# Kernel tuning notes

Hardware: AMD Instinct MI355X
Metric: run time of the kernel (lower is better)

The kernel has to match this reference:

```python
import jax, jax.numpy as jnp
import numpy as np

N_NODES = 100000
N_EDGES = 1600000
N_GRAPHS = 64


def setup_inputs() -> dict:
    key = jax.random.key(0)
    ks = jax.random.split(key, 10)
    x = jax.random.normal(ks[0], (N_NODES, 2), jnp.float32)
    edge_index = jax.random.randint(ks[1], (2, N_EDGES), 0, N_NODES, dtype=jnp.int64)
    batch_index = jnp.sort(jax.random.randint(ks[2], (N_NODES,), 0, N_GRAPHS, dtype=jnp.int64))

    def glorot(k, shape):
        return jax.random.normal(k, shape, jnp.float32) * jnp.sqrt(2.0 / (shape[0] + shape[1]))

    return {
        "x": x,
        "edge_index": edge_index,
        "batch_index": batch_index,
        "W1": glorot(ks[3], (2, 8)),   "b1": jnp.zeros((8,), jnp.float32),
        "W2": glorot(ks[4], (8, 32)),  "b2": jnp.zeros((32,), jnp.float32),
        "W3": glorot(ks[5], (32, 128)),"b3": jnp.zeros((128,), jnp.float32),
        "Wl": glorot(ks[6], (128, 3)), "bl": jnp.zeros((3,), jnp.float32),
    }


def _gcn_conv(x, W, b, src, dst, norm, n):
    # GCNConv: linear transform, then normalized scatter-add aggregation, then bias.
    h = x @ W                                     # [N, out]
    msg = h[src] * norm[:, None]                  # [E', out] gather + scale
    agg = jax.ops.segment_sum(msg, dst, num_segments=n)
    return agg + b


def reference(x, edge_index, batch_index, W1, b1, W2, b2, W3, b3, Wl, bl):
    n = x.shape[0]
    loop = jnp.arange(n, dtype=edge_index.dtype)
    src = jnp.concatenate([edge_index[0], loop])  # add self-loops (GCNConv default)
    dst = jnp.concatenate([edge_index[1], loop])
    # symmetric normalization D^{-1/2} (A+I) D^{-1/2}
    deg = jax.ops.segment_sum(jnp.ones_like(dst, dtype=x.dtype), dst, num_segments=n)
    dis = jnp.where(deg > 0, jax.lax.rsqrt(jnp.maximum(deg, 1.0)), 0.0)
    norm = dis[src] * dis[dst]

    h = jax.nn.relu(_gcn_conv(x, W1, b1, src, dst, norm, n))
    h = jax.nn.relu(_gcn_conv(h, W2, b2, src, dst, norm, n))  # dropout is identity in eval
    h = _gcn_conv(h, W3, b3, src, dst, norm, n)               # [N, 128]
    pooled = jax.ops.segment_max(h, batch_index, num_segments=N_GRAPHS)  # global_max_pool
    logits = pooled @ Wl + bl                                  # [G, 3]
    return jax.nn.log_softmax(logits, axis=1)
```

## Files before the change

### kernel.cpp

```cpp
#include <hip/hip_runtime.h>
#include <hip/hip_fp16.h>


#define BSHIFT 9
#define BSZ 512
#define P2_TILE 2048
#define P1_BLOCKS 128
#define SRCMASK 0x1FFFF
#define NB3 32

__device__ __forceinline__ unsigned fenc(float x) {
  unsigned b = __float_as_uint(x);
  return (b & 0x80000000u) ? ~b : (b | 0x80000000u);
}
__device__ __forceinline__ float fdec(unsigned k) {
  return (k & 0x80000000u) ? __uint_as_float(k ^ 0x80000000u)
                           : __uint_as_float(~k);
}
__device__ __forceinline__ unsigned pack2(float a, float b) {
  __half2 h = __floats2half2_rn(a, b);
  return *reinterpret_cast<unsigned*>(&h);
}
__device__ __forceinline__ float2 unpack2(unsigned u) {
  __half2 h = *reinterpret_cast<__half2*>(&u);
  return __half22float2(h);
}


__global__ __launch_bounds__(256) void p1_hist_kernel(const int* __restrict__ dst,
                                                      int* __restrict__ hist2d, int E) {
  __shared__ int h[256];
  h[threadIdx.x] = 0;
  __syncthreads();
  for (int e = blockIdx.x * blockDim.x + threadIdx.x; e < E; e += gridDim.x * blockDim.x)
    atomicAdd(&h[dst[e] >> BSHIFT], 1);
  __syncthreads();
  hist2d[blockIdx.x * 256 + threadIdx.x] = h[threadIdx.x];
}

__global__ __launch_bounds__(256) void p1_scan_kernel(const int* __restrict__ hist2d,
                                                      int* __restrict__ bucketBase,
                                                      int* __restrict__ bucketCursor,
                                                      unsigned* __restrict__ pooled,
                                                      int B, int E, int G) {
  __shared__ int s[256];
  int t = threadIdx.x;
  int v = 0;
  for (int b = 0; b < P1_BLOCKS; ++b) v += hist2d[b * 256 + t];
  if (t >= B) v = 0;
  s[t] = v;
  __syncthreads();
  for (int o = 1; o < 256; o <<= 1) {
    int u = (t >= o) ? s[t - o] : 0;
    __syncthreads();
    s[t] += u;
    __syncthreads();
  }
  int excl = s[t] - v;
  bucketBase[t] = excl;
  bucketCursor[t] = excl;
  if (t == 0) bucketBase[256] = E;
  for (int i = t; i < G * 128; i += 256) pooled[i] = 0u;
}

__global__ __launch_bounds__(256) void p2_partition_kernel(
    const int* __restrict__ src, const int* __restrict__ dst,
    int* __restrict__ bucketCursor, unsigned* __restrict__ part, int E) {
  __shared__ int hist[256];
  __shared__ int lbase[256];
  __shared__ int gbase[256];
  __shared__ int cur[256];
  __shared__ unsigned sbuf[P2_TILE];
  __shared__ unsigned abuf[P2_TILE];
  int t = threadIdx.x;
  int e0 = blockIdx.x * P2_TILE;
  int cnt = min(P2_TILE, E - e0);

  hist[t] = 0;
  __syncthreads();

  int myb[P2_TILE / 256];
  unsigned myp[P2_TILE / 256];
#pragma unroll
  for (int k = 0; k < P2_TILE / 256; ++k) {
    int i = t + k * 256;
    if (i < cnt) {
      int e = e0 + i;
      int d = dst[e];
      int b = d >> BSHIFT;
      myb[k] = b;
      myp[k] = ((unsigned)(d & (BSZ - 1)) << 17) | (unsigned)src[e];
      atomicAdd(&hist[b], 1);
    } else {
      myb[k] = -1;
      myp[k] = 0;
    }
  }
  __syncthreads();

  int v = hist[t];
  lbase[t] = v;
  __syncthreads();
  for (int o = 1; o < 256; o <<= 1) {
    int u = (t >= o) ? lbase[t - o] : 0;
    __syncthreads();
    lbase[t] += u;
    __syncthreads();
  }
  int excl = lbase[t] - v;
  __syncthreads();
  lbase[t] = excl;
  if (v > 0) gbase[t] = atomicAdd(&bucketCursor[t], v);
  cur[t] = 0;
  __syncthreads();

#pragma unroll
  for (int k = 0; k < P2_TILE / 256; ++k) {
    int b = myb[k];
    if (b >= 0) {
      int pos = atomicAdd(&cur[b], 1);
      int li = lbase[b] + pos;
      sbuf[li] = myp[k];
      abuf[li] = (unsigned)(gbase[b] + pos);
    }
  }
  __syncthreads();

#pragma unroll
  for (int k = 0; k < P2_TILE / 256; ++k) {
    int i = t + k * 256;
    if (i < cnt) part[abuf[i]] = sbuf[i];
  }
}

__global__ __launch_bounds__(512) void p3_build_kernel(
    const unsigned* __restrict__ part, const int* __restrict__ bucketBase,
    const float* __restrict__ x, unsigned* __restrict__ xsh,
    float* __restrict__ dis, int* __restrict__ rp, unsigned* __restrict__ csr,
    int N, int B, int E) {
  __shared__ int hist[BSZ];
  __shared__ int scn[BSZ];
  int b = blockIdx.x, t = threadIdx.x;
  int base = bucketBase[b], end = bucketBase[b + 1];
  int cnt = end - base;

  hist[t] = 0;
  __syncthreads();
  for (int i = t; i < cnt; i += BSZ) atomicAdd(&hist[part[base + i] >> 17], 1);
  __syncthreads();

  int v = hist[t];
  scn[t] = v;
  __syncthreads();
  for (int o = 1; o < BSZ; o <<= 1) {
    int u = (t >= o) ? scn[t - o] : 0;
    __syncthreads();
    scn[t] += u;
    __syncthreads();
  }
  int excl = scn[t] - v;

  int n = (b << BSHIFT) + t;
  if (n < N) {
    float dn = rsqrtf((float)v + 1.0f);
    dis[n] = dn;
    rp[n] = base + excl;
    float2 xn = *reinterpret_cast<const float2*>(x + 2 * (size_t)n);
    xsh[n] = pack2(dn * xn.x, dn * xn.y);
  }
  if (b == B - 1 && t == 0) rp[N] = E;

  hist[t] = excl;
  __syncthreads();
  for (int i = t; i < cnt; i += BSZ) {
    unsigned p = part[base + i];
    int pos = atomicAdd(&hist[p >> 17], 1);
    csr[base + pos] = p & SRCMASK;
  }
}


__global__ __launch_bounds__(256) void layer1_kernel(
    const int* __restrict__ rp, const unsigned* __restrict__ csr, const float* __restrict__ dis,
    const unsigned* __restrict__ xsh, const float* __restrict__ W1, const float* __restrict__ b1,
    uint4* __restrict__ h1h, int N) {
  __shared__ float sW[16];
  __shared__ float sb[8];
  int t = threadIdx.x;
  if (t < 16) sW[t] = W1[t];
  if (t < 8) sb[t] = b1[t];
  __syncthreads();
  int n = blockIdx.x * blockDim.x + t;
  if (n >= N) return;
  float2 a = unpack2(xsh[n]);
  int j0 = rp[n], j1 = rp[n + 1];
#pragma unroll 4
  for (int j = j0; j < j1; ++j) {
    const float2 v = unpack2(xsh[csr[j]]);
    a.x += v.x;
    a.y += v.y;
  }
  float dn = dis[n];
  float ax = dn * a.x, ay = dn * a.y;
  uint4 pk;
  unsigned* pw = &pk.x;
#pragma unroll
  for (int fc = 0; fc < 4; ++fc) {
    float e0 = dn * fmaxf(ax * sW[fc * 2 + 0] + ay * sW[8 + fc * 2 + 0] + sb[fc * 2 + 0], 0.f);
    float e1 = dn * fmaxf(ax * sW[fc * 2 + 1] + ay * sW[8 + fc * 2 + 1] + sb[fc * 2 + 1], 0.f);
    pw[fc] = pack2(e0, e1);
  }
  h1h[n] = pk;
}

__global__ __launch_bounds__(256) void layer2_kernel(
    const int* __restrict__ rp, const unsigned* __restrict__ csr, const float* __restrict__ dis,
    const uint4* __restrict__ h1h, const float* __restrict__ W2, const float* __restrict__ b2,
    __half* __restrict__ h2h, int N) {
  __shared__ float sW[256];
  __shared__ float sb[32];
  int t = threadIdx.x;
  sW[t] = W2[t];
  if (t < 32) sb[t] = b2[t];
  __syncthreads();
  int n = blockIdx.x * blockDim.x + t;
  if (n >= N) return;
  float acc[8];
  {
    uint4 sv = h1h[n];
    float2 f0 = unpack2(sv.x), f1 = unpack2(sv.y), f2 = unpack2(sv.z), f3 = unpack2(sv.w);
    acc[0] = f0.x; acc[1] = f0.y; acc[2] = f1.x; acc[3] = f1.y;
    acc[4] = f2.x; acc[5] = f2.y; acc[6] = f3.x; acc[7] = f3.y;
  }
  int j0 = rp[n], j1 = rp[n + 1];
#pragma unroll 4
  for (int j = j0; j < j1; ++j) {
    uint4 v = h1h[csr[j]];
    float2 g0 = unpack2(v.x), g1 = unpack2(v.y), g2 = unpack2(v.z), g3 = unpack2(v.w);
    acc[0] += g0.x; acc[1] += g0.y; acc[2] += g1.x; acc[3] += g1.y;
    acc[4] += g2.x; acc[5] += g2.y; acc[6] += g3.x; acc[7] += g3.y;
  }
  float dn = dis[n];
#pragma unroll
  for (int k = 0; k < 8; ++k) acc[k] *= dn;
  uint4 pk[4];
  unsigned* pw = &pk[0].x;
#pragma unroll
  for (int fc = 0; fc < 8; ++fc) {
    float4 o;
    o.x = sb[fc * 4 + 0]; o.y = sb[fc * 4 + 1]; o.z = sb[fc * 4 + 2]; o.w = sb[fc * 4 + 3];
#pragma unroll
    for (int k = 0; k < 8; ++k) {
      const float4 w = *reinterpret_cast<const float4*>(&sW[k * 32 + fc * 4]);
      float a = acc[k];
      o.x += a * w.x; o.y += a * w.y; o.z += a * w.z; o.w += a * w.w;
    }
    o.x = dn * fmaxf(o.x, 0.f);
    o.y = dn * fmaxf(o.y, 0.f);
    o.z = dn * fmaxf(o.z, 0.f);
    o.w = dn * fmaxf(o.w, 0.f);
    pw[fc * 2 + 0] = pack2(o.x, o.y);
    pw[fc * 2 + 1] = pack2(o.z, o.w);
  }
  uint4* dst16 = reinterpret_cast<uint4*>(h2h + (size_t)n * 32);
  dst16[0] = pk[0];
  dst16[1] = pk[1];
  dst16[2] = pk[2];
  dst16[3] = pk[3];
}

__global__ __launch_bounds__(128) void layer3_pool_kernel(
    const int* __restrict__ rp, const unsigned* __restrict__ csr, const float* __restrict__ dis,
    const __half* __restrict__ h2h, const float* __restrict__ W3, const float* __restrict__ b3,
    const int* __restrict__ batch, unsigned* __restrict__ pooled, int N) {
  __shared__ float rows[NB3][32];
  __shared__ float dnv[NB3];
  int t = threadIdx.x;
  int gi = t >> 2;
  int q = t & 3;

  int n0 = blockIdx.x * NB3;
  int m = min(NB3, N - n0);

  if (t < m) dnv[t] = dis[n0 + t];

  if (gi < m) {
    int n = n0 + gi;
    uint4 sv = *reinterpret_cast<const uint4*>(h2h + (size_t)n * 32 + q * 8);
    float2 f0 = unpack2(sv.x), f1 = unpack2(sv.y), f2 = unpack2(sv.z), f3 = unpack2(sv.w);
    float acc[8] = {f0.x, f0.y, f1.x, f1.y, f2.x, f2.y, f3.x, f3.y};
    int j0 = rp[n], j1 = rp[n + 1];
#pragma unroll 4
    for (int j = j0; j < j1; ++j) {
      int s = csr[j];
      uint4 v = *reinterpret_cast<const uint4*>(h2h + (size_t)s * 32 + q * 8);
      float2 g0 = unpack2(v.x), g1 = unpack2(v.y), g2 = unpack2(v.z), g3 = unpack2(v.w);
      acc[0] += g0.x; acc[1] += g0.y; acc[2] += g1.x; acc[3] += g1.y;
      acc[4] += g2.x; acc[5] += g2.y; acc[6] += g3.x; acc[7] += g3.y;
    }
#pragma unroll
    for (int i = 0; i < 8; ++i) rows[gi][q * 8 + i] = acc[i];
  }
  __syncthreads();

  float Wreg[32];
#pragma unroll
  for (int k = 0; k < 32; ++k) Wreg[k] = W3[k * 128 + t];
  float bb = b3[t];

  int curg = batch[n0];
  float runmax = -INFINITY;
  for (int r = 0; r < m; ++r) {
    int g = batch[n0 + r];
    if (g != curg) {
      atomicMax(&pooled[(size_t)curg * 128 + t], fenc(runmax));
      runmax = -INFINITY;
      curg = g;
    }
    float acc = 0.f;
#pragma unroll
    for (int k = 0; k < 32; ++k) acc += rows[r][k] * Wreg[k];
    runmax = fmaxf(runmax, dnv[r] * acc + bb);
  }
  atomicMax(&pooled[(size_t)curg * 128 + t], fenc(runmax));
}

__global__ __launch_bounds__(128) void head_kernel(
    const unsigned* __restrict__ pooled, const float* __restrict__ Wl,
    const float* __restrict__ bl, float* __restrict__ out, int G) {
  int g = blockIdx.x;
  int t = threadIdx.x;
  float p = fdec(pooled[(size_t)g * 128 + t]);
  __shared__ float red[128];
  __shared__ float sj[3];
  for (int j = 0; j < 3; ++j) {
    red[t] = p * Wl[t * 3 + j];
    __syncthreads();
    for (int k = 64; k > 0; k >>= 1) {
      if (t < k) red[t] += red[t + k];
      __syncthreads();
    }
    if (t == 0) sj[j] = red[0];
    __syncthreads();
  }
  if (t == 0) {
    float l0 = sj[0] + bl[0], l1 = sj[1] + bl[1], l2 = sj[2] + bl[2];
    float m = fmaxf(l0, fmaxf(l1, l2));
    float lse = logf(expf(l0 - m) + expf(l1 - m) + expf(l2 - m));
    out[g * 3 + 0] = l0 - m - lse;
    out[g * 3 + 1] = l1 - m - lse;
    out[g * 3 + 2] = l2 - m - lse;
  }
}

extern "C" void kernel_launch(void* const* d_in, const int* in_sizes, int n_in,
                              void* d_out, int out_size, void* d_ws, size_t ws_size,
                              hipStream_t stream) {
  const float* x = (const float*)d_in[0];
  const int* ei = (const int*)d_in[1];
  const int* batch = (const int*)d_in[2];
  const float* W1 = (const float*)d_in[3];
  const float* b1 = (const float*)d_in[4];
  const float* W2 = (const float*)d_in[5];
  const float* b2 = (const float*)d_in[6];
  const float* W3 = (const float*)d_in[7];
  const float* b3 = (const float*)d_in[8];
  const float* Wl = (const float*)d_in[9];
  const float* bl = (const float*)d_in[10];
  float* out = (float*)d_out;

  const int N = in_sizes[0] / 2;
  const int E = in_sizes[1] / 2;
  const int G = out_size / 3;

  const int* src = ei;
  const int* dstp = ei + E;

  const int B = (N + BSZ - 1) / BSZ;

  size_t NP = ((size_t)N + 256) & ~(size_t)255;
  size_t EP = ((size_t)E + 255) & ~(size_t)255;

  float* dis = (float*)d_ws;
  int* rp = (int*)d_ws + NP;
  unsigned* csr = (unsigned*)(rp + NP);
  unsigned* part = (unsigned*)(csr + EP);
  int* bucketBase = (int*)(part + EP);
  int* bucketCursor = bucketBase + 512;
  int* hist2d = bucketCursor + 512;
  float* arena = (float*)(hist2d + P1_BLOCKS * 256);

  unsigned* xsh = (unsigned*)arena;
  uint4* h1h = (uint4*)(arena + (size_t)N);
  __half* h2h = (__half*)(arena + (size_t)5 * N);
  unsigned* pooled = (unsigned*)(arena + (size_t)21 * N);

  const int BS = 256;
  auto cdiv = [](long long a, long long b) { return (int)((a + b - 1) / b); };

  p1_hist_kernel<<<P1_BLOCKS, 256, 0, stream>>>(dstp, hist2d, E);
  p1_scan_kernel<<<1, 256, 0, stream>>>(hist2d, bucketBase, bucketCursor, pooled, B, E, G);
  p2_partition_kernel<<<cdiv(E, P2_TILE), 256, 0, stream>>>(src, dstp, bucketCursor, part, E);
  p3_build_kernel<<<B, BSZ, 0, stream>>>(part, bucketBase, x, xsh, dis, rp, csr, N, B, E);

  layer1_kernel<<<cdiv(N, BS), BS, 0, stream>>>(rp, csr, dis, xsh, W1, b1, h1h, N);
  layer2_kernel<<<cdiv(N, BS), BS, 0, stream>>>(rp, csr, dis, h1h, W2, b2, h2h, N);
  layer3_pool_kernel<<<cdiv(N, NB3), 128, 0, stream>>>(rp, csr, dis, h2h, W3, b3, batch, pooled, N);

  head_kernel<<<G, 128, 0, stream>>>(pooled, Wl, bl, out, G);
}
```

Baseline: 134.1 us.

## Sort nodes by degree within each bucket to balance warp work in layers 1-2

The CSR build kernel now computes a per-bucket counting sort of nodes by in-degree (capped at 63) and writes a permutation array. Layers 1 and 2 process nodes in that permuted order so that lanes in a wavefront have similar neighbor-loop trip counts, reducing divergence from uneven degrees. In exchange, per-node loads and stores (rp, xsh, h1h, dis) become less coalesced because neighboring threads now touch scattered node indices, and the build kernel gains extra shared atomics and a serial scan.

```diff
diff --git a/kernel.cpp b/kernel.cpp
--- a/kernel.cpp
+++ b/kernel.cpp
@@ -137,9 +137,11 @@
     const unsigned* __restrict__ part, const int* __restrict__ bucketBase,
     const float* __restrict__ x, unsigned* __restrict__ xsh,
     float* __restrict__ dis, int* __restrict__ rp, unsigned* __restrict__ csr,
-    int N, int B, int E) {
+    int* __restrict__ perm, int N, int B, int E) {
   __shared__ int hist[BSZ];
   __shared__ int scn[BSZ];
+  __shared__ int dh[64];
+  __shared__ int dc[64];
   int b = blockIdx.x, t = threadIdx.x;
   int base = bucketBase[b], end = bucketBase[b + 1];
   int cnt = end - base;
@@ -171,17 +173,36 @@
   if (b == B - 1 && t == 0) rp[N] = E;
 
   hist[t] = excl;
+  if (t < 64) dh[t] = 0;
   __syncthreads();
   for (int i = t; i < cnt; i += BSZ) {
     unsigned p = part[base + i];
     int pos = atomicAdd(&hist[p >> 17], 1);
     csr[base + pos] = p & SRCMASK;
   }
+
+  int bin = min(v, 63);
+  if (n < N) atomicAdd(&dh[bin], 1);
+  __syncthreads();
+  if (t == 0) {
+    int run = 0;
+#pragma unroll
+    for (int i = 0; i < 64; ++i) {
+      dc[i] = run;
+      run += dh[i];
+    }
+  }
+  __syncthreads();
+  if (n < N) {
+    int pos = atomicAdd(&dc[bin], 1);
+    perm[(b << BSHIFT) + pos] = n;
+  }
 }
 
 
 __global__ __launch_bounds__(256) void layer1_kernel(
     const int* __restrict__ rp, const unsigned* __restrict__ csr, const float* __restrict__ dis,
+    const int* __restrict__ perm,
     const unsigned* __restrict__ xsh, const float* __restrict__ W1, const float* __restrict__ b1,
     uint4* __restrict__ h1h, int N) {
   __shared__ float sW[16];
@@ -190,8 +211,9 @@
   if (t < 16) sW[t] = W1[t];
   if (t < 8) sb[t] = b1[t];
   __syncthreads();
-  int n = blockIdx.x * blockDim.x + t;
-  if (n >= N) return;
+  int tid = blockIdx.x * blockDim.x + t;
+  if (tid >= N) return;
+  int n = perm[tid];
   float2 a = unpack2(xsh[n]);
   int j0 = rp[n], j1 = rp[n + 1];
 #pragma unroll 4
@@ -215,6 +237,7 @@
 
 __global__ __launch_bounds__(256) void layer2_kernel(
     const int* __restrict__ rp, const unsigned* __restrict__ csr, const float* __restrict__ dis,
+    const int* __restrict__ perm,
     const uint4* __restrict__ h1h, const float* __restrict__ W2, const float* __restrict__ b2,
     __half* __restrict__ h2h, int N) {
   __shared__ float sW[256];
@@ -223,8 +246,9 @@
   sW[t] = W2[t];
   if (t < 32) sb[t] = b2[t];
   __syncthreads();
-  int n = blockIdx.x * blockDim.x + t;
-  if (n >= N) return;
+  int tid = blockIdx.x * blockDim.x + t;
+  if (tid >= N) return;
+  int n = perm[tid];
   float acc[8];
   {
     uint4 sv = h1h[n];
@@ -388,7 +412,8 @@
   int* bucketBase = (int*)(part + EP);
   int* bucketCursor = bucketBase + 512;
   int* hist2d = bucketCursor + 512;
-  float* arena = (float*)(hist2d + P1_BLOCKS * 256);
+  int* perm = hist2d + P1_BLOCKS * 256;
+  float* arena = (float*)(perm + NP);
 
   unsigned* xsh = (unsigned*)arena;
   uint4* h1h = (uint4*)(arena + (size_t)N);
@@ -401,10 +426,10 @@
   p1_hist_kernel<<<P1_BLOCKS, 256, 0, stream>>>(dstp, hist2d, E);
   p1_scan_kernel<<<1, 256, 0, stream>>>(hist2d, bucketBase, bucketCursor, pooled, B, E, G);
   p2_partition_kernel<<<cdiv(E, P2_TILE), 256, 0, stream>>>(src, dstp, bucketCursor, part, E);
-  p3_build_kernel<<<B, BSZ, 0, stream>>>(part, bucketBase, x, xsh, dis, rp, csr, N, B, E);
-
-  layer1_kernel<<<cdiv(N, BS), BS, 0, stream>>>(rp, csr, dis, xsh, W1, b1, h1h, N);
-  layer2_kernel<<<cdiv(N, BS), BS, 0, stream>>>(rp, csr, dis, h1h, W2, b2, h2h, N);
+  p3_build_kernel<<<B, BSZ, 0, stream>>>(part, bucketBase, x, xsh, dis, rp, csr, perm, N, B, E);
+
+  layer1_kernel<<<cdiv(N, BS), BS, 0, stream>>>(rp, csr, dis, perm, xsh, W1, b1, h1h, N);
+  layer2_kernel<<<cdiv(N, BS), BS, 0, stream>>>(rp, csr, dis, perm, h1h, W2, b2, h2h, N);
   layer3_pool_kernel<<<cdiv(N, NB3), 128, 0, stream>>>(rp, csr, dis, h2h, W3, b3, batch, pooled, N);
 
   head_kernel<<<G, 128, 0, stream>>>(pooled, Wl, bl, out, G);
```

Measured after the change: 138.9 us. +3.5%, slower.

## Replace dst histogram pass with fixed-capacity bucket regions in partition

Applied to the files above, without the earlier changes.

Drops the separate histogram and scan kernels that read all destination indices before partitioning. The partition kernel now writes each bucket into its own fixed-capacity region (CAP slots) using an atomic per-bucket count. A small scan over those counts then gives CSR offsets, and a memset zeroes the counters and the pooled buffer. This saves a full pass over the edge array and one launch, but assumes no bucket exceeds CAP edges, which holds only for roughly uniform destination distributions. It also enlarges the workspace.

```diff
diff --git a/kernel.cpp b/kernel.cpp
--- a/kernel.cpp
+++ b/kernel.cpp
@@ -5,7 +5,7 @@
 #define BSHIFT 9
 #define BSZ 512
 #define P2_TILE 2048
-#define P1_BLOCKS 128
+#define CAP 16384
 #define SRCMASK 0x1FFFF
 #define NB3 32
 
@@ -27,45 +27,9 @@
 }
 
 
-__global__ __launch_bounds__(256) void p1_hist_kernel(const int* __restrict__ dst,
-                                                      int* __restrict__ hist2d, int E) {
-  __shared__ int h[256];
-  h[threadIdx.x] = 0;
-  __syncthreads();
-  for (int e = blockIdx.x * blockDim.x + threadIdx.x; e < E; e += gridDim.x * blockDim.x)
-    atomicAdd(&h[dst[e] >> BSHIFT], 1);
-  __syncthreads();
-  hist2d[blockIdx.x * 256 + threadIdx.x] = h[threadIdx.x];
-}
-
-__global__ __launch_bounds__(256) void p1_scan_kernel(const int* __restrict__ hist2d,
-                                                      int* __restrict__ bucketBase,
-                                                      int* __restrict__ bucketCursor,
-                                                      unsigned* __restrict__ pooled,
-                                                      int B, int E, int G) {
-  __shared__ int s[256];
-  int t = threadIdx.x;
-  int v = 0;
-  for (int b = 0; b < P1_BLOCKS; ++b) v += hist2d[b * 256 + t];
-  if (t >= B) v = 0;
-  s[t] = v;
-  __syncthreads();
-  for (int o = 1; o < 256; o <<= 1) {
-    int u = (t >= o) ? s[t - o] : 0;
-    __syncthreads();
-    s[t] += u;
-    __syncthreads();
-  }
-  int excl = s[t] - v;
-  bucketBase[t] = excl;
-  bucketCursor[t] = excl;
-  if (t == 0) bucketBase[256] = E;
-  for (int i = t; i < G * 128; i += 256) pooled[i] = 0u;
-}
-
 __global__ __launch_bounds__(256) void p2_partition_kernel(
     const int* __restrict__ src, const int* __restrict__ dst,
-    int* __restrict__ bucketCursor, unsigned* __restrict__ part, int E) {
+    int* __restrict__ bucketCount, unsigned* __restrict__ part, int E) {
   __shared__ int hist[256];
   __shared__ int lbase[256];
   __shared__ int gbase[256];
@@ -110,7 +74,7 @@
   int excl = lbase[t] - v;
   __syncthreads();
   lbase[t] = excl;
-  if (v > 0) gbase[t] = atomicAdd(&bucketCursor[t], v);
+  if (v > 0) gbase[t] = atomicAdd(&bucketCount[t], v);
   cur[t] = 0;
   __syncthreads();
 
@@ -121,7 +85,7 @@
       int pos = atomicAdd(&cur[b], 1);
       int li = lbase[b] + pos;
       sbuf[li] = myp[k];
-      abuf[li] = (unsigned)(gbase[b] + pos);
+      abuf[li] = (unsigned)(b * CAP + gbase[b] + pos);
     }
   }
   __syncthreads();
@@ -133,20 +97,38 @@
   }
 }
 
+__global__ __launch_bounds__(256) void scan_kernel(const int* __restrict__ bucketCount,
+                                                   int* __restrict__ bucketBase, int B) {
+  __shared__ int s[256];
+  int t = threadIdx.x;
+  int v = (t < B) ? bucketCount[t] : 0;
+  s[t] = v;
+  __syncthreads();
+  for (int o = 1; o < 256; o <<= 1) {
+    int u = (t >= o) ? s[t - o] : 0;
+    __syncthreads();
+    s[t] += u;
+    __syncthreads();
+  }
+  bucketBase[t] = s[t] - v;
+}
+
 __global__ __launch_bounds__(512) void p3_build_kernel(
-    const unsigned* __restrict__ part, const int* __restrict__ bucketBase,
+    const unsigned* __restrict__ part, const int* __restrict__ bucketCount,
+    const int* __restrict__ bucketBase,
     const float* __restrict__ x, unsigned* __restrict__ xsh,
     float* __restrict__ dis, int* __restrict__ rp, unsigned* __restrict__ csr,
     int N, int B, int E) {
   __shared__ int hist[BSZ];
   __shared__ int scn[BSZ];
   int b = blockIdx.x, t = threadIdx.x;
-  int base = bucketBase[b], end = bucketBase[b + 1];
-  int cnt = end - base;
+  const unsigned* reg = part + (size_t)b * CAP;
+  int cnt = bucketCount[b];
+  int wbase = bucketBase[b];
 
   hist[t] = 0;
   __syncthreads();
-  for (int i = t; i < cnt; i += BSZ) atomicAdd(&hist[part[base + i] >> 17], 1);
+  for (int i = t; i < cnt; i += BSZ) atomicAdd(&hist[reg[i] >> 17], 1);
   __syncthreads();
 
   int v = hist[t];
@@ -164,7 +146,7 @@
   if (n < N) {
     float dn = rsqrtf((float)v + 1.0f);
     dis[n] = dn;
-    rp[n] = base + excl;
+    rp[n] = wbase + excl;
     float2 xn = *reinterpret_cast<const float2*>(x + 2 * (size_t)n);
     xsh[n] = pack2(dn * xn.x, dn * xn.y);
   }
@@ -173,9 +155,9 @@
   hist[t] = excl;
   __syncthreads();
   for (int i = t; i < cnt; i += BSZ) {
-    unsigned p = part[base + i];
+    unsigned p = reg[i];
     int pos = atomicAdd(&hist[p >> 17], 1);
-    csr[base + pos] = p & SRCMASK;
+    csr[wbase + pos] = p & SRCMASK;
   }
 }
 
@@ -385,23 +367,23 @@
   int* rp = (int*)d_ws + NP;
   unsigned* csr = (unsigned*)(rp + NP);
   unsigned* part = (unsigned*)(csr + EP);
-  int* bucketBase = (int*)(part + EP);
-  int* bucketCursor = bucketBase + 512;
-  int* hist2d = bucketCursor + 512;
-  float* arena = (float*)(hist2d + P1_BLOCKS * 256);
+  int* ctrl = (int*)(part + (size_t)256 * CAP);
+  int* bucketCount = ctrl;
+  unsigned* pooled = (unsigned*)(ctrl + 256);
+  int* bucketBase = (int*)(pooled + (size_t)G * 128);
+  float* arena = (float*)(bucketBase + 256);
 
   unsigned* xsh = (unsigned*)arena;
   uint4* h1h = (uint4*)(arena + (size_t)N);
   __half* h2h = (__half*)(arena + (size_t)5 * N);
-  unsigned* pooled = (unsigned*)(arena + (size_t)21 * N);
 
   const int BS = 256;
   auto cdiv = [](long long a, long long b) { return (int)((a + b - 1) / b); };
 
-  p1_hist_kernel<<<P1_BLOCKS, 256, 0, stream>>>(dstp, hist2d, E);
-  p1_scan_kernel<<<1, 256, 0, stream>>>(hist2d, bucketBase, bucketCursor, pooled, B, E, G);
-  p2_partition_kernel<<<cdiv(E, P2_TILE), 256, 0, stream>>>(src, dstp, bucketCursor, part, E);
-  p3_build_kernel<<<B, BSZ, 0, stream>>>(part, bucketBase, x, xsh, dis, rp, csr, N, B, E);
+  hipMemsetAsync(ctrl, 0, (256 + (size_t)G * 128) * 4, stream);
+  p2_partition_kernel<<<cdiv(E, P2_TILE), 256, 0, stream>>>(src, dstp, bucketCount, part, E);
+  scan_kernel<<<1, 256, 0, stream>>>(bucketCount, bucketBase, B);
+  p3_build_kernel<<<B, BSZ, 0, stream>>>(part, bucketCount, bucketBase, x, xsh, dis, rp, csr, N, B, E);
 
   layer1_kernel<<<cdiv(N, BS), BS, 0, stream>>>(rp, csr, dis, xsh, W1, b1, h1h, N);
   layer2_kernel<<<cdiv(N, BS), BS, 0, stream>>>(rp, csr, dis, h1h, W2, b2, h2h, N);
```

Result: faster. 119.0 us (-11.3%).
